# Performance work log

Hardware: AMD Instinct MI355X
Metric: run time of the kernel (lower is better)

Reference implementation:

```python
import jax, jax.numpy as jnp
import numpy as np

N = 50000
E = 400000
F_IN = 128
NUM_CLASSES = 16
# (heads, out_channels, concat) per GATConv layer
LAYERS = [(8, 32, True), (8, 16, True), (8, 8, True), (1, NUM_CLASSES, False)]
DIMS_IN = [F_IN, 256, 128, 64]
NEG_SLOPE = 0.2
BN_EPS = 1e-5


def setup_inputs() -> dict:
    key = jax.random.key(0)
    ks = iter(jax.random.split(key, 64))
    inp = {}
    inp["x"] = jax.random.normal(next(ks), (N, F_IN), dtype=jnp.float32)
    inp["src"] = jax.random.randint(next(ks), (E,), 0, N, dtype=jnp.int32)
    inp["dst"] = jax.random.randint(next(ks), (E,), 0, N, dtype=jnp.int32)
    for l, ((h, c, concat), din) in enumerate(zip(LAYERS, DIMS_IN), start=1):
        s = 1.0 / np.sqrt(din)
        inp[f"W{l}"] = jax.random.normal(next(ks), (din, h * c), dtype=jnp.float32) * s
        inp[f"asrc{l}"] = jax.random.normal(next(ks), (h, c), dtype=jnp.float32) * 0.1
        inp[f"adst{l}"] = jax.random.normal(next(ks), (h, c), dtype=jnp.float32) * 0.1
        dout = h * c if concat else c
        inp[f"b{l}"] = jax.random.normal(next(ks), (dout,), dtype=jnp.float32) * 0.01
        inp[f"g{l}"] = jax.random.uniform(next(ks), (dout,), dtype=jnp.float32, minval=0.5, maxval=1.5)
        inp[f"be{l}"] = jax.random.normal(next(ks), (dout,), dtype=jnp.float32) * 0.1
        inp[f"rm{l}"] = jax.random.normal(next(ks), (dout,), dtype=jnp.float32) * 0.1
        inp[f"rv{l}"] = jax.random.uniform(next(ks), (dout,), dtype=jnp.float32, minval=0.5, maxval=1.5)
    return inp


def _gat_conv(x, src, dst, W, a_src, a_dst, bias, heads, ch, concat):
    n = x.shape[0]
    h = (x @ W).reshape(n, heads, ch)                     # [N,H,C]
    e_s = jnp.einsum('nhc,hc->nh', h, a_src)              # [N,H]
    e_d = jnp.einsum('nhc,hc->nh', h, a_dst)
    alpha = jax.nn.leaky_relu(e_s[src] + e_d[dst], NEG_SLOPE)   # [E,H]
    amax = jax.ops.segment_max(alpha, dst, num_segments=n)
    ex = jnp.exp(alpha - amax[dst])
    den = jax.ops.segment_sum(ex, dst, num_segments=n)
    attn = ex / (den[dst] + 1e-16)                        # [E,H]
    out = jax.ops.segment_sum(h[src] * attn[:, :, None], dst, num_segments=n)  # [N,H,C]
    out = out.reshape(n, heads * ch) if concat else out.mean(axis=1)
    return out + bias


def _bn(x, g, b, rm, rv):
    return (x - rm) * jax.lax.rsqrt(rv + BN_EPS) * g + b


def _forward(x, src, dst, params):
    # PyG GATConv adds self-loops by default
    loops = jnp.arange(N, dtype=src.dtype)
    s = jnp.concatenate([src, loops])
    d = jnp.concatenate([dst, loops])
    out = x
    for l, (h, c, concat) in enumerate(LAYERS, start=1):
        W, a_s, a_d, b, g, be, rm, rv = (params[f"{k}{l}"] for k in
                                         ("W", "asrc", "adst", "b", "g", "be", "rm", "rv"))
        out = _gat_conv(out, s, d, W, a_s, a_d, b, h, c, concat)
        if l < 4:
            out = jax.nn.elu(out)
        out = _bn(out, g, be, rm, rv)
    return out


def reference(x, src, dst,
              W1, asrc1, adst1, b1, g1, be1, rm1, rv1,
              W2, asrc2, adst2, b2, g2, be2, rm2, rv2,
              W3, asrc3, adst3, b3, g3, be3, rm3, rv3,
              W4, asrc4, adst4, b4, g4, be4, rm4, rv4):
    params = dict(
        W1=W1, asrc1=asrc1, adst1=adst1, b1=b1, g1=g1, be1=be1, rm1=rm1, rv1=rv1,
        W2=W2, asrc2=asrc2, adst2=adst2, b2=b2, g2=g2, be2=be2, rm2=rm2, rv2=rv2,
        W3=W3, asrc3=asrc3, adst3=adst3, b3=b3, g3=g3, be3=be3, rm3=rm3, rv3=rv3,
        W4=W4, asrc4=asrc4, adst4=adst4, b4=b4, g4=g4, be4=be4, rm4=rm4, rv4=rv4)
    return _forward(x, src, dst, params)
```

## Files before the change

kernel.cpp:

```cpp
#include <hip/hip_runtime.h>

#define NEG_SLOPE 0.2f
#define BN_EPS 1e-5f

typedef unsigned short u16;
typedef unsigned int u32;
typedef __bf16 bf16x8 __attribute__((ext_vector_type(8)));
typedef float f32x4 __attribute__((ext_vector_type(4)));

__device__ __forceinline__ u32 f2bf(float f) {
    u32 u = __float_as_uint(f);
    return (u + 0x7FFFu + ((u >> 16) & 1u)) >> 16;
}
__device__ __forceinline__ float bf2f(u32 h) { return __uint_as_float(h << 16); }
__device__ __forceinline__ float bfl(u32 p) { return __uint_as_float(p << 16); }
__device__ __forceinline__ float bfh(u32 p) { return __uint_as_float(p & 0xFFFF0000u); }

__device__ __forceinline__ void split8(const float4 f0, const float4 f1, uint4& vh, uint4& vl) {
    float f[8] = {f0.x, f0.y, f0.z, f0.w, f1.x, f1.y, f1.z, f1.w};
    u32 h[8], l[8];
    #pragma unroll
    for (int i = 0; i < 8; i++) { h[i] = f2bf(f[i]); l[i] = f2bf(f[i] - bf2f(h[i])); }
    vh = make_uint4(h[0] | (h[1] << 16), h[2] | (h[3] << 16), h[4] | (h[5] << 16), h[6] | (h[7] << 16));
    vl = make_uint4(l[0] | (l[1] << 16), l[2] | (l[3] << 16), l[4] | (l[5] << 16), l[6] | (l[7] << 16));
}

__global__ void wt_prep3(const float* __restrict__ W1, const float* __restrict__ W2,
                         const float* __restrict__ W3,
                         u16* __restrict__ h1, u16* __restrict__ l1,
                         u16* __restrict__ h2, u16* __restrict__ l2,
                         u16* __restrict__ h3, u16* __restrict__ l3) {
    int i = blockIdx.x * blockDim.x + threadIdx.x;
    const float* W; u16 *ph, *pl; int K, N, off;
    if (i < 32768)      { W = W1; ph = h1; pl = l1; K = 128; N = 256; off = i; }
    else if (i < 65536) { W = W2; ph = h2; pl = l2; K = 256; N = 128; off = i - 32768; }
    else if (i < 73728) { W = W3; ph = h3; pl = l3; K = 128; N = 64;  off = i - 65536; }
    else return;
    int k = off / N, n = off - k * N;
    float w = W[off];
    u32 h = f2bf(w);
    ph[n * K + k] = (u16)h;
    pl[n * K + k] = (u16)f2bf(w - bf2f(h));
}

template<int BN, int HMC, int AF32>
__launch_bounds__(256)
__global__ void gemm_mfma(const void* __restrict__ A_, const u16* __restrict__ Alo,
                          const u16* __restrict__ Bhi, const u16* __restrict__ Blo,
                          u16* __restrict__ Cbf, int M, int K, int N) {
    constexpr int FM = (BN == 128) ? 4 : 2;
    __shared__ uint4 sA[2][512];
    __shared__ uint4 sB[2][BN * 4];
    const int tid = threadIdx.x;
    const int bm = blockIdx.y * 128;
    const int bn = blockIdx.x * BN;
    const int lane = tid & 63;
    const int w = tid >> 6;
    const int wm = (BN == 128) ? (w >> 1) * 64 : w * 32;
    const int wn = (BN == 128) ? (w & 1) * 64 : 0;
    const int fr = lane & 15;
    const int fs = lane >> 4;
    f32x4 zero = {0.f, 0.f, 0.f, 0.f};
    f32x4 acc[FM][4];
    #pragma unroll
    for (int i = 0; i < FM; i++)
        #pragma unroll
        for (int j = 0; j < 4; j++) acc[i][j] = zero;

    const int r0 = tid >> 2;
    const int ss = tid & 3;
    const int r1 = r0 + 64;
    const int d0 = r0 * 4 + (ss ^ ((r0 >> 1) & 3));
    const int d1 = r1 * 4 + (ss ^ ((r1 >> 1) & 3));

    for (int k0 = 0; k0 < K; k0 += 32) {
        if constexpr (AF32) {
            const float* Af = (const float*)A_;
            int gr = bm + r0;
            uint4 vh = make_uint4(0,0,0,0), vl = make_uint4(0,0,0,0);
            if (gr < M) {
                float4 f0 = *(const float4*)(Af + (size_t)gr * K + k0 + ss * 8);
                float4 f1 = *(const float4*)(Af + (size_t)gr * K + k0 + ss * 8 + 4);
                split8(f0, f1, vh, vl);
            }
            sA[0][d0] = vh; sA[1][d0] = vl;
            gr = bm + r1;
            vh = make_uint4(0,0,0,0); vl = make_uint4(0,0,0,0);
            if (gr < M) {
                float4 f0 = *(const float4*)(Af + (size_t)gr * K + k0 + ss * 8);
                float4 f1 = *(const float4*)(Af + (size_t)gr * K + k0 + ss * 8 + 4);
                split8(f0, f1, vh, vl);
            }
            sA[0][d1] = vh; sA[1][d1] = vl;
        } else {
            const u16* Ahi = (const u16*)A_;
            int gr = bm + r0;
            uint4 vh = make_uint4(0,0,0,0), vl = make_uint4(0,0,0,0);
            if (gr < M) {
                vh = *(const uint4*)(Ahi + (size_t)gr * K + k0 + ss * 8);
                vl = *(const uint4*)(Alo + (size_t)gr * K + k0 + ss * 8);
            }
            sA[0][d0] = vh; sA[1][d0] = vl;
            gr = bm + r1;
            vh = make_uint4(0,0,0,0); vl = make_uint4(0,0,0,0);
            if (gr < M) {
                vh = *(const uint4*)(Ahi + (size_t)gr * K + k0 + ss * 8);
                vl = *(const uint4*)(Alo + (size_t)gr * K + k0 + ss * 8);
            }
            sA[0][d1] = vh; sA[1][d1] = vl;
        }
        {
            int gr = bn + r0;
            sB[0][d0] = *(const uint4*)(Bhi + (size_t)gr * K + k0 + ss * 8);
            sB[1][d0] = *(const uint4*)(Blo + (size_t)gr * K + k0 + ss * 8);
            if constexpr (BN == 128) {
                gr = bn + r1;
                sB[0][d1] = *(const uint4*)(Bhi + (size_t)gr * K + k0 + ss * 8);
                sB[1][d1] = *(const uint4*)(Blo + (size_t)gr * K + k0 + ss * 8);
            }
        }
        __syncthreads();
        bf16x8 ah[FM], al[FM], bh[4], bl[4];
        #pragma unroll
        for (int mi = 0; mi < FM; mi++) {
            int row = wm + mi * 16 + fr;
            int idx = row * 4 + (fs ^ ((row >> 1) & 3));
            ah[mi] = *reinterpret_cast<const bf16x8*>(&sA[0][idx]);
            al[mi] = *reinterpret_cast<const bf16x8*>(&sA[1][idx]);
        }
        #pragma unroll
        for (int ni = 0; ni < 4; ni++) {
            int row = wn + ni * 16 + fr;
            int idx = row * 4 + (fs ^ ((row >> 1) & 3));
            bh[ni] = *reinterpret_cast<const bf16x8*>(&sB[0][idx]);
            bl[ni] = *reinterpret_cast<const bf16x8*>(&sB[1][idx]);
        }
        #pragma unroll
        for (int mi = 0; mi < FM; mi++)
            #pragma unroll
            for (int ni = 0; ni < 4; ni++) {
                acc[mi][ni] = __builtin_amdgcn_mfma_f32_16x16x32_bf16(ah[mi], bh[ni], acc[mi][ni], 0, 0, 0);
                acc[mi][ni] = __builtin_amdgcn_mfma_f32_16x16x32_bf16(ah[mi], bl[ni], acc[mi][ni], 0, 0, 0);
                acc[mi][ni] = __builtin_amdgcn_mfma_f32_16x16x32_bf16(al[mi], bh[ni], acc[mi][ni], 0, 0, 0);
            }
        __syncthreads();
    }
    #pragma unroll
    for (int mi = 0; mi < FM; mi++) {
        #pragma unroll
        for (int ni = 0; ni < 4; ni++) {
            int colg = bn + wn + ni * 16 + fr;
            int rbase = bm + wm + mi * 16 + fs * 4;
            #pragma unroll
            for (int r = 0; r < 4; r++) {
                int rw = rbase + r;
                if (rw >= M) continue;
                u16 val = (u16)f2bf(acc[mi][ni][r]);
                if constexpr (HMC > 0) {
                    int hh2 = colg / HMC, cc2 = colg - hh2 * HMC;
                    Cbf[((size_t)hh2 * M + rw) * HMC + cc2] = val;
                } else {
                    Cbf[(size_t)rw * N + colg] = val;
                }
            }
        }
    }
}

__launch_bounds__(256)
__global__ void gemm_k64n16(const float* __restrict__ A, const float* __restrict__ B,
                            u16* __restrict__ Cbf, int M) {
    __shared__ float As[64][68];
    __shared__ float Bs[64][16];
    const int tid = threadIdx.x;
    const int bm = blockIdx.x * 64;
    {
        int r = tid >> 2, c = (tid & 3) << 2;
        *reinterpret_cast<float4*>(&Bs[r][c]) = *reinterpret_cast<const float4*>(&B[r * 16 + c]);
    }
    #pragma unroll
    for (int p = 0; p < 4; p++) {
        int m = (tid >> 4) + p * 16;
        int c = (tid & 15) << 2;
        int gm = bm + m;
        float4 v = make_float4(0.f, 0.f, 0.f, 0.f);
        if (gm < M) v = *reinterpret_cast<const float4*>(&A[(size_t)gm * 64 + c]);
        *reinterpret_cast<float4*>(&As[m][c]) = v;
    }
    __syncthreads();
    const int tc = tid & 15;
    const int r0 = tid >> 4;
    float acc[4] = {};
    #pragma unroll
    for (int k4 = 0; k4 < 16; k4++) {
        float b0 = Bs[4 * k4 + 0][tc];
        float b1 = Bs[4 * k4 + 1][tc];
        float b2 = Bs[4 * k4 + 2][tc];
        float b3 = Bs[4 * k4 + 3][tc];
        #pragma unroll
        for (int i = 0; i < 4; i++) {
            float4 av = *reinterpret_cast<const float4*>(&As[r0 + i * 16][4 * k4]);
            acc[i] += av.x * b0 + av.y * b1 + av.z * b2 + av.w * b3;
        }
    }
    #pragma unroll
    for (int i = 0; i < 4; i++) {
        int m = bm + r0 + i * 16;
        if (m < M) Cbf[(size_t)m * 16 + tc] = (u16)f2bf(acc[i]);
    }
}

__global__ void scores_kernel(const u16* __restrict__ h,
                              const float* __restrict__ asrc,
                              const float* __restrict__ adst,
                              float* __restrict__ es, float* __restrict__ ed,
                              int Nn, int H, int C) {
    int idx = blockIdx.x * blockDim.x + threadIdx.x;
    if (idx >= Nn * H) return;
    int n = idx / H, hh = idx % H;
    const u16* hp = h + ((size_t)hh * Nn + n) * C;
    const float4* ap = reinterpret_cast<const float4*>(asrc + hh * C);
    const float4* bp = reinterpret_cast<const float4*>(adst + hh * C);
    float s = 0.f, d = 0.f;
    for (int c4 = 0; c4 < C / 4; c4++) {
        uint2 pv = *reinterpret_cast<const uint2*>(hp + 4 * c4);
        float v0 = bfl(pv.x), v1 = bfh(pv.x), v2 = bfl(pv.y), v3 = bfh(pv.y);
        float4 a = ap[c4], b = bp[c4];
        s += v0 * a.x + v1 * a.y + v2 * a.z + v3 * a.w;
        d += v0 * b.x + v1 * b.y + v2 * b.z + v3 * b.w;
    }
    es[(size_t)hh * Nn + n] = s;
    ed[(size_t)hh * Nn + n] = d;
}

__global__ void hist_kernel(const int* __restrict__ dst, int* __restrict__ counts,
                            int E0, int Etot) {
    int e = blockIdx.x * blockDim.x + threadIdx.x;
    if (e >= Etot) return;
    int d_ = (e < E0) ? dst[e] : e - E0;
    atomicAdd(&counts[d_], 1);
}

__global__ void scan_kernel(int* __restrict__ counts, int* __restrict__ row_ptr, int Nn) {
    __shared__ int wsum[16];
    __shared__ int chunk_total;
    __shared__ int carry_s;
    const int tid = threadIdx.x;
    const int lane = tid & 63;
    const int wid = tid >> 6;
    if (tid == 0) carry_s = 0;
    __syncthreads();
    for (int base = 0; base < Nn; base += 1024) {
        int i = base + tid;
        int v = (i < Nn) ? counts[i] : 0;
        int iv = v;
        #pragma unroll
        for (int off = 1; off < 64; off <<= 1) {
            int t = __shfl_up(iv, off, 64);
            if (lane >= off) iv += t;
        }
        if (lane == 63) wsum[wid] = iv;
        __syncthreads();
        if (tid == 0) {
            int s = 0;
            #pragma unroll
            for (int k = 0; k < 16; k++) { int t = wsum[k]; wsum[k] = s; s += t; }
            chunk_total = s;
        }
        __syncthreads();
        if (i < Nn) {
            int ex = carry_s + wsum[wid] + (iv - v);
            row_ptr[i] = ex;
            counts[i] = ex;
        }
        __syncthreads();
        if (tid == 0) carry_s += chunk_total;
        __syncthreads();
    }
    if (tid == 0) row_ptr[Nn] = carry_s;
}

__global__ void scatter_kernel(const int* __restrict__ src, const int* __restrict__ dst,
                               int* __restrict__ cursor, int* __restrict__ col,
                               int E0, int Etot) {
    int e = blockIdx.x * blockDim.x + threadIdx.x;
    if (e >= Etot) return;
    int d_ = (e < E0) ? dst[e] : e - E0;
    int s_ = (e < E0) ? src[e] : e - E0;
    int pos = atomicAdd(&cursor[d_], 1);
    col[pos] = s_;
}

template<int H, int C, int NT, int DO_ELU, int OUT_HILO>
__launch_bounds__(256)
__global__ void gat_fused(const int* __restrict__ row_ptr, const int* __restrict__ col,
                          const float* __restrict__ es, const float* __restrict__ ed,
                          const u16* __restrict__ h16, float* __restrict__ outf,
                          u16* __restrict__ outh, u16* __restrict__ outl,
                          const float* __restrict__ bias, const float* __restrict__ g,
                          const float* __restrict__ be, const float* __restrict__ rm,
                          const float* __restrict__ rv, int Nn) {
    constexpr int Dout = H * C;
    constexpr int VEC = C / NT;
    constexpr int NPB = 256 / NT;
    const int tid = threadIdx.x;
    const int node = blockIdx.x * NPB + tid / NT;
    const int t = tid % NT;
    const int hh = blockIdx.y;
    if (node >= Nn) return;
    const int jb = row_ptr[node], je = row_ptr[node + 1];
    const float* esh = es + (size_t)hh * Nn;
    const float edv = ed[(size_t)hh * Nn + node];
    const u16* hb = h16 + (size_t)hh * Nn * C + t * VEC;
    float acc[VEC] = {};
    float den = 0.f;
    int j = jb;
    for (; j + 4 <= je; j += 4) {
        int s0 = col[j], s1 = col[j + 1], s2 = col[j + 2], s3 = col[j + 3];
        float e0 = esh[s0] + edv, e1 = esh[s1] + edv, e2 = esh[s2] + edv, e3 = esh[s3] + edv;
        e0 = (e0 >= 0.f) ? e0 : NEG_SLOPE * e0;
        e1 = (e1 >= 0.f) ? e1 : NEG_SLOPE * e1;
        e2 = (e2 >= 0.f) ? e2 : NEG_SLOPE * e2;
        e3 = (e3 >= 0.f) ? e3 : NEG_SLOPE * e3;
        float w0 = __expf(e0), w1 = __expf(e1), w2 = __expf(e2), w3 = __expf(e3);
        den += (w0 + w1) + (w2 + w3);
        if constexpr (VEC == 8) {
            uint4 p0 = *reinterpret_cast<const uint4*>(hb + (size_t)s0 * C);
            uint4 p1 = *reinterpret_cast<const uint4*>(hb + (size_t)s1 * C);
            uint4 p2 = *reinterpret_cast<const uint4*>(hb + (size_t)s2 * C);
            uint4 p3 = *reinterpret_cast<const uint4*>(hb + (size_t)s3 * C);
            acc[0] += w0 * bfl(p0.x) + w1 * bfl(p1.x) + w2 * bfl(p2.x) + w3 * bfl(p3.x);
            acc[1] += w0 * bfh(p0.x) + w1 * bfh(p1.x) + w2 * bfh(p2.x) + w3 * bfh(p3.x);
            acc[2] += w0 * bfl(p0.y) + w1 * bfl(p1.y) + w2 * bfl(p2.y) + w3 * bfl(p3.y);
            acc[3] += w0 * bfh(p0.y) + w1 * bfh(p1.y) + w2 * bfh(p2.y) + w3 * bfh(p3.y);
            acc[4] += w0 * bfl(p0.z) + w1 * bfl(p1.z) + w2 * bfl(p2.z) + w3 * bfl(p3.z);
            acc[5] += w0 * bfh(p0.z) + w1 * bfh(p1.z) + w2 * bfh(p2.z) + w3 * bfh(p3.z);
            acc[6] += w0 * bfl(p0.w) + w1 * bfl(p1.w) + w2 * bfl(p2.w) + w3 * bfl(p3.w);
            acc[7] += w0 * bfh(p0.w) + w1 * bfh(p1.w) + w2 * bfh(p2.w) + w3 * bfh(p3.w);
        } else {
            uint2 p0 = *reinterpret_cast<const uint2*>(hb + (size_t)s0 * C);
            uint2 p1 = *reinterpret_cast<const uint2*>(hb + (size_t)s1 * C);
            uint2 p2 = *reinterpret_cast<const uint2*>(hb + (size_t)s2 * C);
            uint2 p3 = *reinterpret_cast<const uint2*>(hb + (size_t)s3 * C);
            acc[0] += w0 * bfl(p0.x) + w1 * bfl(p1.x) + w2 * bfl(p2.x) + w3 * bfl(p3.x);
            acc[1] += w0 * bfh(p0.x) + w1 * bfh(p1.x) + w2 * bfh(p2.x) + w3 * bfh(p3.x);
            acc[2] += w0 * bfl(p0.y) + w1 * bfl(p1.y) + w2 * bfl(p2.y) + w3 * bfl(p3.y);
            acc[3] += w0 * bfh(p0.y) + w1 * bfh(p1.y) + w2 * bfh(p2.y) + w3 * bfh(p3.y);
        }
    }
    for (; j < je; j++) {
        int s = col[j];
        float a = esh[s] + edv;
        a = (a >= 0.f) ? a : NEG_SLOPE * a;
        float w = __expf(a);
        den += w;
        if constexpr (VEC == 8) {
            uint4 pv = *reinterpret_cast<const uint4*>(hb + (size_t)s * C);
            acc[0] += w * bfl(pv.x); acc[1] += w * bfh(pv.x);
            acc[2] += w * bfl(pv.y); acc[3] += w * bfh(pv.y);
            acc[4] += w * bfl(pv.z); acc[5] += w * bfh(pv.z);
            acc[6] += w * bfl(pv.w); acc[7] += w * bfh(pv.w);
        } else {
            uint2 pv = *reinterpret_cast<const uint2*>(hb + (size_t)s * C);
            acc[0] += w * bfl(pv.x); acc[1] += w * bfh(pv.x);
            acc[2] += w * bfl(pv.y); acc[3] += w * bfh(pv.y);
        }
    }
    const float inv = 1.f / (den + 1e-16f);
    const int jc = hh * C + t * VEC;
    float res[VEC];
    #pragma unroll
    for (int v = 0; v < VEC; v++) {
        float y = acc[v] * inv + bias[jc + v];
        if (DO_ELU) y = (y > 0.f) ? y : expm1f(y);
        y = (y - rm[jc + v]) * rsqrtf(rv[jc + v] + BN_EPS) * g[jc + v] + be[jc + v];
        res[v] = y;
    }
    if constexpr (OUT_HILO) {
        u32 rh[VEC], rl[VEC];
        #pragma unroll
        for (int v = 0; v < VEC; v++) {
            rh[v] = f2bf(res[v]);
            rl[v] = f2bf(res[v] - bf2f(rh[v]));
        }
        if constexpr (VEC == 8) {
            uint4 ph = make_uint4(rh[0] | (rh[1] << 16), rh[2] | (rh[3] << 16),
                                  rh[4] | (rh[5] << 16), rh[6] | (rh[7] << 16));
            uint4 pl = make_uint4(rl[0] | (rl[1] << 16), rl[2] | (rl[3] << 16),
                                  rl[4] | (rl[5] << 16), rl[6] | (rl[7] << 16));
            *reinterpret_cast<uint4*>(outh + (size_t)node * Dout + jc) = ph;
            *reinterpret_cast<uint4*>(outl + (size_t)node * Dout + jc) = pl;
        } else {
            uint2 ph = make_uint2(rh[0] | (rh[1] << 16), rh[2] | (rh[3] << 16));
            uint2 pl = make_uint2(rl[0] | (rl[1] << 16), rl[2] | (rl[3] << 16));
            *reinterpret_cast<uint2*>(outh + (size_t)node * Dout + jc) = ph;
            *reinterpret_cast<uint2*>(outl + (size_t)node * Dout + jc) = pl;
        }
    } else {
        float* op = outf + (size_t)node * Dout + jc;
        if constexpr (VEC == 8) {
            *reinterpret_cast<float4*>(op) = make_float4(res[0], res[1], res[2], res[3]);
            *reinterpret_cast<float4*>(op + 4) = make_float4(res[4], res[5], res[6], res[7]);
        } else {
            *reinterpret_cast<float4*>(op) = make_float4(res[0], res[1], res[2], res[3]);
        }
    }
}

extern "C" void kernel_launch(void* const* d_in, const int* in_sizes, int n_in,
                              void* d_out, int out_size, void* d_ws, size_t ws_size,
                              hipStream_t stream) {
    const float* x = (const float*)d_in[0];
    const int* src = (const int*)d_in[1];
    const int* dst = (const int*)d_in[2];
    const int Nn = in_sizes[0] / 128;
    const int E0 = in_sizes[1];
    const int Etot = E0 + Nn;

    u16* A0 = (u16*)d_ws;
    u16* Bh = A0 + (size_t)Nn * 512;
    u16* Ch = Bh + (size_t)Nn * 256;
    float* es = (float*)(Ch + (size_t)Nn * 256);
    float* ed = es + (size_t)Nn * 8;
    int* row_ptr = (int*)(ed + (size_t)Nn * 8);
    int* cursor  = row_ptr + (Nn + 1);
    int* col     = cursor + Nn;
    u16* wth1 = (u16*)(col + Etot);
    u16* wtl1 = wth1 + 32768;
    u16* wth2 = wtl1 + 32768;
    u16* wtl2 = wth2 + 32768;
    u16* wth3 = wtl2 + 32768;
    u16* wtl3 = wth3 + 8192;

    u16* Y1H = A0;
    u16* Y1L = A0 + (size_t)Nn * 256;
    u16* Y2H = Ch;
    u16* Y2L = Ch + (size_t)Nn * 128;
    float* out3 = (float*)A0;

    hipMemsetAsync(cursor, 0, sizeof(int) * Nn, stream);
    hist_kernel<<<(Etot + 255) / 256, 256, 0, stream>>>(dst, cursor, E0, Etot);
    scan_kernel<<<1, 1024, 0, stream>>>(cursor, row_ptr, Nn);
    scatter_kernel<<<(Etot + 255) / 256, 256, 0, stream>>>(src, dst, cursor, col, E0, Etot);

    const int gy128 = (Nn + 127) / 128;

    const float* const* p1 = (const float* const*)(d_in + 3);
    const float* const* p2 = (const float* const*)(d_in + 11);
    const float* const* p3 = (const float* const*)(d_in + 19);
    const float* const* p4 = (const float* const*)(d_in + 27);

    wt_prep3<<<288, 256, 0, stream>>>(p1[0], p2[0], p3[0], wth1, wtl1, wth2, wtl2, wth3, wtl3);

    gemm_mfma<128, 32, 1><<<dim3(2, gy128), 256, 0, stream>>>(x, nullptr, wth1, wtl1, Bh, Nn, 128, 256);
    scores_kernel<<<(Nn * 8 + 255) / 256, 256, 0, stream>>>(Bh, p1[1], p1[2], es, ed, Nn, 8, 32);
    gat_fused<8, 32, 4, 1, 1><<<dim3((Nn + 63) / 64, 8), 256, 0, stream>>>(
        row_ptr, col, es, ed, Bh, nullptr, Y1H, Y1L, p1[3], p1[4], p1[5], p1[6], p1[7], Nn);

    gemm_mfma<128, 16, 0><<<dim3(1, gy128), 256, 0, stream>>>(Y1H, Y1L, wth2, wtl2, Bh, Nn, 256, 128);
    scores_kernel<<<(Nn * 8 + 255) / 256, 256, 0, stream>>>(Bh, p2[1], p2[2], es, ed, Nn, 8, 16);
    gat_fused<8, 16, 2, 1, 1><<<dim3((Nn + 127) / 128, 8), 256, 0, stream>>>(
        row_ptr, col, es, ed, Bh, nullptr, Y2H, Y2L, p2[3], p2[4], p2[5], p2[6], p2[7], Nn);

    gemm_mfma<64, 8, 0><<<dim3(1, gy128), 256, 0, stream>>>(Y2H, Y2L, wth3, wtl3, Bh, Nn, 128, 64);
    scores_kernel<<<(Nn * 8 + 255) / 256, 256, 0, stream>>>(Bh, p3[1], p3[2], es, ed, Nn, 8, 8);
    gat_fused<8, 8, 2, 1, 0><<<dim3((Nn + 127) / 128, 8), 256, 0, stream>>>(
        row_ptr, col, es, ed, Bh, out3, nullptr, nullptr, p3[3], p3[4], p3[5], p3[6], p3[7], Nn);

    gemm_k64n16<<<(Nn + 63) / 64, 256, 0, stream>>>(out3, p4[0], Bh, Nn);
    scores_kernel<<<(Nn + 255) / 256, 256, 0, stream>>>(Bh, p4[1], p4[2], es, ed, Nn, 1, 16);
    gat_fused<1, 16, 2, 0, 0><<<dim3((Nn + 127) / 128, 1), 256, 0, stream>>>(
        row_ptr, col, es, ed, Bh, (float*)d_out, nullptr, nullptr, p4[3], p4[4], p4[5], p4[6], p4[7], Nn);
}
```

Baseline: 400.5 us.

## Switch hidden features to node-major layout and aggregate all heads per node group

The GEMM now writes hidden features row-major as [N, H*C] rather than head-major as [H, N, C], and the attention scores move to [N, H]. The fused aggregation kernel now gives each node a group of threads that covers every head at once, with each thread handling 8 channels. The neighbour index list is then read once per node instead of once per head, and each neighbour row becomes one contiguous gather. The trade-off is larger groups per node, so work can become imbalanced when node degrees vary, and the per-head score reads inside a group are strided.

```diff
diff --git a/kernel.cpp b/kernel.cpp
--- a/kernel.cpp
+++ b/kernel.cpp
@@ -43,7 +43,7 @@
     pl[n * K + k] = (u16)f2bf(w - bf2f(h));
 }
 
-template<int BN, int HMC, int AF32>
+template<int BN, int AF32>
 __launch_bounds__(256)
 __global__ void gemm_mfma(const void* __restrict__ A_, const u16* __restrict__ Alo,
                           const u16* __restrict__ Bhi, const u16* __restrict__ Blo,
@@ -154,14 +154,7 @@
             #pragma unroll
             for (int r = 0; r < 4; r++) {
                 int rw = rbase + r;
-                if (rw >= M) continue;
-                u16 val = (u16)f2bf(acc[mi][ni][r]);
-                if constexpr (HMC > 0) {
-                    int hh2 = colg / HMC, cc2 = colg - hh2 * HMC;
-                    Cbf[((size_t)hh2 * M + rw) * HMC + cc2] = val;
-                } else {
-                    Cbf[(size_t)rw * N + colg] = val;
-                }
+                if (rw < M) Cbf[(size_t)rw * N + colg] = (u16)f2bf(acc[mi][ni][r]);
             }
         }
     }
@@ -218,7 +211,7 @@
     int idx = blockIdx.x * blockDim.x + threadIdx.x;
     if (idx >= Nn * H) return;
     int n = idx / H, hh = idx % H;
-    const u16* hp = h + ((size_t)hh * Nn + n) * C;
+    const u16* hp = h + (size_t)n * (H * C) + hh * C;
     const float4* ap = reinterpret_cast<const float4*>(asrc + hh * C);
     const float4* bp = reinterpret_cast<const float4*>(adst + hh * C);
     float s = 0.f, d = 0.f;
@@ -229,8 +222,8 @@
         s += v0 * a.x + v1 * a.y + v2 * a.z + v3 * a.w;
         d += v0 * b.x + v1 * b.y + v2 * b.z + v3 * b.w;
     }
-    es[(size_t)hh * Nn + n] = s;
-    ed[(size_t)hh * Nn + n] = d;
+    es[(size_t)n * H + hh] = s;
+    ed[(size_t)n * H + hh] = d;
 }
 
 __global__ void hist_kernel(const int* __restrict__ dst, int* __restrict__ counts,
@@ -291,7 +284,7 @@
     col[pos] = s_;
 }
 
-template<int H, int C, int NT, int DO_ELU, int OUT_HILO>
+template<int H, int C, int G, int DO_ELU, int OUT_HILO>
 __launch_bounds__(256)
 __global__ void gat_fused(const int* __restrict__ row_ptr, const int* __restrict__ col,
                           const float* __restrict__ es, const float* __restrict__ ed,
@@ -301,109 +294,84 @@
                           const float* __restrict__ be, const float* __restrict__ rm,
                           const float* __restrict__ rv, int Nn) {
     constexpr int Dout = H * C;
-    constexpr int VEC = C / NT;
-    constexpr int NPB = 256 / NT;
+    constexpr int VEC = 8;
+    static_assert(G * VEC == Dout, "group must cover the row");
+    constexpr int NPB = 256 / G;
     const int tid = threadIdx.x;
-    const int node = blockIdx.x * NPB + tid / NT;
-    const int t = tid % NT;
-    const int hh = blockIdx.y;
+    const int node = blockIdx.x * NPB + tid / G;
+    const int t = tid % G;
     if (node >= Nn) return;
+    const int hh = (t * VEC) / C;
     const int jb = row_ptr[node], je = row_ptr[node + 1];
-    const float* esh = es + (size_t)hh * Nn;
-    const float edv = ed[(size_t)hh * Nn + node];
-    const u16* hb = h16 + (size_t)hh * Nn * C + t * VEC;
-    float acc[VEC] = {};
+    const float edv = ed[(size_t)node * H + hh];
+    const u16* hb = h16 + t * VEC;
+    float acc[8] = {};
     float den = 0.f;
     int j = jb;
     for (; j + 4 <= je; j += 4) {
         int s0 = col[j], s1 = col[j + 1], s2 = col[j + 2], s3 = col[j + 3];
-        float e0 = esh[s0] + edv, e1 = esh[s1] + edv, e2 = esh[s2] + edv, e3 = esh[s3] + edv;
+        uint4 p0 = *reinterpret_cast<const uint4*>(hb + (size_t)s0 * Dout);
+        uint4 p1 = *reinterpret_cast<const uint4*>(hb + (size_t)s1 * Dout);
+        uint4 p2 = *reinterpret_cast<const uint4*>(hb + (size_t)s2 * Dout);
+        uint4 p3 = *reinterpret_cast<const uint4*>(hb + (size_t)s3 * Dout);
+        float e0 = es[(size_t)s0 * H + hh] + edv;
+        float e1 = es[(size_t)s1 * H + hh] + edv;
+        float e2 = es[(size_t)s2 * H + hh] + edv;
+        float e3 = es[(size_t)s3 * H + hh] + edv;
         e0 = (e0 >= 0.f) ? e0 : NEG_SLOPE * e0;
         e1 = (e1 >= 0.f) ? e1 : NEG_SLOPE * e1;
         e2 = (e2 >= 0.f) ? e2 : NEG_SLOPE * e2;
         e3 = (e3 >= 0.f) ? e3 : NEG_SLOPE * e3;
         float w0 = __expf(e0), w1 = __expf(e1), w2 = __expf(e2), w3 = __expf(e3);
         den += (w0 + w1) + (w2 + w3);
-        if constexpr (VEC == 8) {
-            uint4 p0 = *reinterpret_cast<const uint4*>(hb + (size_t)s0 * C);
-            uint4 p1 = *reinterpret_cast<const uint4*>(hb + (size_t)s1 * C);
-            uint4 p2 = *reinterpret_cast<const uint4*>(hb + (size_t)s2 * C);
-            uint4 p3 = *reinterpret_cast<const uint4*>(hb + (size_t)s3 * C);
-            acc[0] += w0 * bfl(p0.x) + w1 * bfl(p1.x) + w2 * bfl(p2.x) + w3 * bfl(p3.x);
-            acc[1] += w0 * bfh(p0.x) + w1 * bfh(p1.x) + w2 * bfh(p2.x) + w3 * bfh(p3.x);
-            acc[2] += w0 * bfl(p0.y) + w1 * bfl(p1.y) + w2 * bfl(p2.y) + w3 * bfl(p3.y);
-            acc[3] += w0 * bfh(p0.y) + w1 * bfh(p1.y) + w2 * bfh(p2.y) + w3 * bfh(p3.y);
-            acc[4] += w0 * bfl(p0.z) + w1 * bfl(p1.z) + w2 * bfl(p2.z) + w3 * bfl(p3.z);
-            acc[5] += w0 * bfh(p0.z) + w1 * bfh(p1.z) + w2 * bfh(p2.z) + w3 * bfh(p3.z);
-            acc[6] += w0 * bfl(p0.w) + w1 * bfl(p1.w) + w2 * bfl(p2.w) + w3 * bfl(p3.w);
-            acc[7] += w0 * bfh(p0.w) + w1 * bfh(p1.w) + w2 * bfh(p2.w) + w3 * bfh(p3.w);
-        } else {
-            uint2 p0 = *reinterpret_cast<const uint2*>(hb + (size_t)s0 * C);
-            uint2 p1 = *reinterpret_cast<const uint2*>(hb + (size_t)s1 * C);
-            uint2 p2 = *reinterpret_cast<const uint2*>(hb + (size_t)s2 * C);
-            uint2 p3 = *reinterpret_cast<const uint2*>(hb + (size_t)s3 * C);
-            acc[0] += w0 * bfl(p0.x) + w1 * bfl(p1.x) + w2 * bfl(p2.x) + w3 * bfl(p3.x);
-            acc[1] += w0 * bfh(p0.x) + w1 * bfh(p1.x) + w2 * bfh(p2.x) + w3 * bfh(p3.x);
-            acc[2] += w0 * bfl(p0.y) + w1 * bfl(p1.y) + w2 * bfl(p2.y) + w3 * bfl(p3.y);
-            acc[3] += w0 * bfh(p0.y) + w1 * bfh(p1.y) + w2 * bfh(p2.y) + w3 * bfh(p3.y);
-        }
+        acc[0] += w0 * bfl(p0.x) + w1 * bfl(p1.x) + w2 * bfl(p2.x) + w3 * bfl(p3.x);
+        acc[1] += w0 * bfh(p0.x) + w1 * bfh(p1.x) + w2 * bfh(p2.x) + w3 * bfh(p3.x);
+        acc[2] += w0 * bfl(p0.y) + w1 * bfl(p1.y) + w2 * bfl(p2.y) + w3 * bfl(p3.y);
+        acc[3] += w0 * bfh(p0.y) + w1 * bfh(p1.y) + w2 * bfh(p2.y) + w3 * bfh(p3.y);
+        acc[4] += w0 * bfl(p0.z) + w1 * bfl(p1.z) + w2 * bfl(p2.z) + w3 * bfl(p3.z);
+        acc[5] += w0 * bfh(p0.z) + w1 * bfh(p1.z) + w2 * bfh(p2.z) + w3 * bfh(p3.z);
+        acc[6] += w0 * bfl(p0.w) + w1 * bfl(p1.w) + w2 * bfl(p2.w) + w3 * bfl(p3.w);
+        acc[7] += w0 * bfh(p0.w) + w1 * bfh(p1.w) + w2 * bfh(p2.w) + w3 * bfh(p3.w);
     }
     for (; j < je; j++) {
         int s = col[j];
-        float a = esh[s] + edv;
+        uint4 pv = *reinterpret_cast<const uint4*>(hb + (size_t)s * Dout);
+        float a = es[(size_t)s * H + hh] + edv;
         a = (a >= 0.f) ? a : NEG_SLOPE * a;
         float w = __expf(a);
         den += w;
-        if constexpr (VEC == 8) {
-            uint4 pv = *reinterpret_cast<const uint4*>(hb + (size_t)s * C);
-            acc[0] += w * bfl(pv.x); acc[1] += w * bfh(pv.x);
-            acc[2] += w * bfl(pv.y); acc[3] += w * bfh(pv.y);
-            acc[4] += w * bfl(pv.z); acc[5] += w * bfh(pv.z);
-            acc[6] += w * bfl(pv.w); acc[7] += w * bfh(pv.w);
-        } else {
-            uint2 pv = *reinterpret_cast<const uint2*>(hb + (size_t)s * C);
-            acc[0] += w * bfl(pv.x); acc[1] += w * bfh(pv.x);
-            acc[2] += w * bfl(pv.y); acc[3] += w * bfh(pv.y);
-        }
+        acc[0] += w * bfl(pv.x); acc[1] += w * bfh(pv.x);
+        acc[2] += w * bfl(pv.y); acc[3] += w * bfh(pv.y);
+        acc[4] += w * bfl(pv.z); acc[5] += w * bfh(pv.z);
+        acc[6] += w * bfl(pv.w); acc[7] += w * bfh(pv.w);
     }
     const float inv = 1.f / (den + 1e-16f);
-    const int jc = hh * C + t * VEC;
-    float res[VEC];
-    #pragma unroll
-    for (int v = 0; v < VEC; v++) {
+    const int jc = t * VEC;
+    float res[8];
+    #pragma unroll
+    for (int v = 0; v < 8; v++) {
         float y = acc[v] * inv + bias[jc + v];
         if (DO_ELU) y = (y > 0.f) ? y : expm1f(y);
         y = (y - rm[jc + v]) * rsqrtf(rv[jc + v] + BN_EPS) * g[jc + v] + be[jc + v];
         res[v] = y;
     }
     if constexpr (OUT_HILO) {
-        u32 rh[VEC], rl[VEC];
-        #pragma unroll
-        for (int v = 0; v < VEC; v++) {
+        u32 rh[8], rl[8];
+        #pragma unroll
+        for (int v = 0; v < 8; v++) {
             rh[v] = f2bf(res[v]);
             rl[v] = f2bf(res[v] - bf2f(rh[v]));
         }
-        if constexpr (VEC == 8) {
-            uint4 ph = make_uint4(rh[0] | (rh[1] << 16), rh[2] | (rh[3] << 16),
-                                  rh[4] | (rh[5] << 16), rh[6] | (rh[7] << 16));
-            uint4 pl = make_uint4(rl[0] | (rl[1] << 16), rl[2] | (rl[3] << 16),
-                                  rl[4] | (rl[5] << 16), rl[6] | (rl[7] << 16));
-            *reinterpret_cast<uint4*>(outh + (size_t)node * Dout + jc) = ph;
-            *reinterpret_cast<uint4*>(outl + (size_t)node * Dout + jc) = pl;
-        } else {
-            uint2 ph = make_uint2(rh[0] | (rh[1] << 16), rh[2] | (rh[3] << 16));
-            uint2 pl = make_uint2(rl[0] | (rl[1] << 16), rl[2] | (rl[3] << 16));
-            *reinterpret_cast<uint2*>(outh + (size_t)node * Dout + jc) = ph;
-            *reinterpret_cast<uint2*>(outl + (size_t)node * Dout + jc) = pl;
-        }
+        uint4 ph = make_uint4(rh[0] | (rh[1] << 16), rh[2] | (rh[3] << 16),
+                              rh[4] | (rh[5] << 16), rh[6] | (rh[7] << 16));
+        uint4 pl = make_uint4(rl[0] | (rl[1] << 16), rl[2] | (rl[3] << 16),
+                              rl[4] | (rl[5] << 16), rl[6] | (rl[7] << 16));
+        *reinterpret_cast<uint4*>(outh + (size_t)node * Dout + jc) = ph;
+        *reinterpret_cast<uint4*>(outl + (size_t)node * Dout + jc) = pl;
     } else {
         float* op = outf + (size_t)node * Dout + jc;
-        if constexpr (VEC == 8) {
-            *reinterpret_cast<float4*>(op) = make_float4(res[0], res[1], res[2], res[3]);
-            *reinterpret_cast<float4*>(op + 4) = make_float4(res[4], res[5], res[6], res[7]);
-        } else {
-            *reinterpret_cast<float4*>(op) = make_float4(res[0], res[1], res[2], res[3]);
-        }
+        *reinterpret_cast<float4*>(op) = make_float4(res[0], res[1], res[2], res[3]);
+        *reinterpret_cast<float4*>(op + 4) = make_float4(res[4], res[5], res[6], res[7]);
     }
 }
 
@@ -452,23 +420,23 @@
 
     wt_prep3<<<288, 256, 0, stream>>>(p1[0], p2[0], p3[0], wth1, wtl1, wth2, wtl2, wth3, wtl3);
 
-    gemm_mfma<128, 32, 1><<<dim3(2, gy128), 256, 0, stream>>>(x, nullptr, wth1, wtl1, Bh, Nn, 128, 256);
+    gemm_mfma<128, 1><<<dim3(2, gy128), 256, 0, stream>>>(x, nullptr, wth1, wtl1, Bh, Nn, 128, 256);
     scores_kernel<<<(Nn * 8 + 255) / 256, 256, 0, stream>>>(Bh, p1[1], p1[2], es, ed, Nn, 8, 32);
-    gat_fused<8, 32, 4, 1, 1><<<dim3((Nn + 63) / 64, 8), 256, 0, stream>>>(
+    gat_fused<8, 32, 32, 1, 1><<<(Nn + 7) / 8, 256, 0, stream>>>(
         row_ptr, col, es, ed, Bh, nullptr, Y1H, Y1L, p1[3], p1[4], p1[5], p1[6], p1[7], Nn);
 
-    gemm_mfma<128, 16, 0><<<dim3(1, gy128), 256, 0, stream>>>(Y1H, Y1L, wth2, wtl2, Bh, Nn, 256, 128);
+    gemm_mfma<128, 0><<<dim3(1, gy128), 256, 0, stream>>>(Y1H, Y1L, wth2, wtl2, Bh, Nn, 256, 128);
     scores_kernel<<<(Nn * 8 + 255) / 256, 256, 0, stream>>>(Bh, p2[1], p2[2], es, ed, Nn, 8, 16);
-    gat_fused<8, 16, 2, 1, 1><<<dim3((Nn + 127) / 128, 8), 256, 0, stream>>>(
+    gat_fused<8, 16, 16, 1, 1><<<(Nn + 15) / 16, 256, 0, stream>>>(
         row_ptr, col, es, ed, Bh, nullptr, Y2H, Y2L, p2[3], p2[4], p2[5], p2[6], p2[7], Nn);
 
-    gemm_mfma<64, 8, 0><<<dim3(1, gy128), 256, 0, stream>>>(Y2H, Y2L, wth3, wtl3, Bh, Nn, 128, 64);
+    gemm_mfma<64, 0><<<dim3(1, gy128), 256, 0, stream>>>(Y2H, Y2L, wth3, wtl3, Bh, Nn, 128, 64);
     scores_kernel<<<(Nn * 8 + 255) / 256, 256, 0, stream>>>(Bh, p3[1], p3[2], es, ed, Nn, 8, 8);
-    gat_fused<8, 8, 2, 1, 0><<<dim3((Nn + 127) / 128, 8), 256, 0, stream>>>(
+    gat_fused<8, 8, 8, 1, 0><<<(Nn + 31) / 32, 256, 0, stream>>>(
         row_ptr, col, es, ed, Bh, out3, nullptr, nullptr, p3[3], p3[4], p3[5], p3[6], p3[7], Nn);
 
     gemm_k64n16<<<(Nn + 63) / 64, 256, 0, stream>>>(out3, p4[0], Bh, Nn);
     scores_kernel<<<(Nn + 255) / 256, 256, 0, stream>>>(Bh, p4[1], p4[2], es, ed, Nn, 1, 16);
-    gat_fused<1, 16, 2, 0, 0><<<dim3((Nn + 127) / 128, 1), 256, 0, stream>>>(
+    gat_fused<1, 16, 2, 0, 0><<<(Nn + 127) / 128, 256, 0, stream>>>(
         row_ptr, col, es, ed, Bh, (float*)d_out, nullptr, nullptr, p4[3], p4[4], p4[5], p4[6], p4[7], Nn);
 }
```

Result: slower. 453.2 us (+13.2%).
